# Kernel tuning notes

Hardware: AMD Instinct MI355X
Metric: run time of the kernel (lower is better)

Reference implementation:

```python
import jax, jax.numpy as jnp
import numpy as np


def setup_inputs() -> dict:
    key = jax.random.key(0)
    k1, k2, k3, k4 = jax.random.split(key, 4)
    N, E, DIN, H1, H2 = 100000, 1600000, 128, 64, 32
    x = jax.random.normal(k1, (N, DIN), dtype=jnp.float32)
    edge_index = jax.random.randint(k2, (2, E), 0, N, dtype=jnp.int64)
    # Glorot-style scaled init for the two GCN weight matrices (no bias)
    W1 = jax.random.normal(k3, (DIN, H1), dtype=jnp.float32) * (1.0 / np.sqrt(DIN))
    W2 = jax.random.normal(k4, (H1, H2), dtype=jnp.float32) * (1.0 / np.sqrt(H1))
    return {"x": x, "edge_index": edge_index, "W1": W1, "W2": W2}


def reference(x, edge_index, W1, W2):
    N = x.shape[0]
    loop = jnp.arange(N, dtype=edge_index.dtype)
    src = jnp.concatenate([edge_index[0], loop])  # [E+N]
    dst = jnp.concatenate([edge_index[1], loop])  # [E+N]
    # symmetric GCN normalization with self-loops (edge_weight = 1)
    deg = jax.ops.segment_sum(jnp.ones(src.shape, x.dtype), dst, num_segments=N)
    dinv = jnp.where(deg > 0, jax.lax.rsqrt(deg), 0.0)
    norm = dinv[src] * dinv[dst]  # [E+N]

    def gcn_conv(h, W):
        h = h @ W  # transform first (PyG GCNConv order)
        msg = h[src] * norm[:, None]  # gather + scale
        return jax.ops.segment_sum(msg, dst, num_segments=N)  # scatter-add

    hidden1 = jax.nn.relu(gcn_conv(x, W1))
    z = gcn_conv(hidden1, W2)
    return z
```

## Files before the change

### kernel.cpp

```cpp
#include <hip/hip_runtime.h>
#include <hip/hip_fp16.h>

#define DIN 128
#define H1  64
#define H2  32
#define NCH 512
#define BSH 8

typedef _Float16 f16x8 __attribute__((ext_vector_type(8)));
typedef _Float16 f16x4 __attribute__((ext_vector_type(4)));
typedef float    f32x4 __attribute__((ext_vector_type(4)));

__global__ __launch_bounds__(256) void k_hist(const int* __restrict__ dst,
        int* __restrict__ H, int E, int NB, int chunk) {
    __shared__ int lh[512];
    int c = blockIdx.x, tid = threadIdx.x;
    for (int b = tid; b < NB; b += 256) lh[b] = 0;
    __syncthreads();
    int e0 = c * chunk, e1 = min(E, e0 + chunk);
    for (int e = e0 + tid; e < e1; e += 256)
        atomicAdd(&lh[dst[e] >> BSH], 1);
    __syncthreads();
    for (int b = tid; b < NB; b += 256) H[(size_t)b * NCH + c] = lh[b];
}

__global__ __launch_bounds__(256) void k_scan1(const int* __restrict__ in,
        int* __restrict__ out, int* __restrict__ partial, int N) {
    int tid = threadIdx.x;
    int base = blockIdx.x * 1024 + tid * 4;
    int v0 = (base + 0 < N) ? in[base + 0] : 0;
    int v1 = (base + 1 < N) ? in[base + 1] : 0;
    int v2 = (base + 2 < N) ? in[base + 2] : 0;
    int v3 = (base + 3 < N) ? in[base + 3] : 0;
    int sum = v0 + v1 + v2 + v3;
    int lane = tid & 63, wid = tid >> 6;
    int x = sum;
#pragma unroll
    for (int off = 1; off < 64; off <<= 1) {
        int y = __shfl_up(x, off, 64);
        if (lane >= off) x += y;
    }
    __shared__ int wsum[4];
    if (lane == 63) wsum[wid] = x;
    __syncthreads();
    int wbase = 0;
    for (int w = 0; w < wid; ++w) wbase += wsum[w];
    int excl = wbase + x - sum;
    if (base + 0 < N) out[base + 0] = excl;
    if (base + 1 < N) out[base + 1] = excl + v0;
    if (base + 2 < N) out[base + 2] = excl + v0 + v1;
    if (base + 3 < N) out[base + 3] = excl + v0 + v1 + v2;
    if (tid == 0) partial[blockIdx.x] = wsum[0] + wsum[1] + wsum[2] + wsum[3];
}

__global__ __launch_bounds__(256) void k_scan2(int* __restrict__ partial, int nb) {
    int tid = threadIdx.x;
    int v = (tid < nb) ? partial[tid] : 0;
    __shared__ int tmp[256];
    tmp[tid] = v;
    __syncthreads();
    for (int off = 1; off < 256; off <<= 1) {
        int y = (tid >= off) ? tmp[tid - off] : 0;
        __syncthreads();
        tmp[tid] += y;
        __syncthreads();
    }
    if (tid < nb) partial[tid] = tmp[tid] - v;
}

__global__ void k_scan3b(int* __restrict__ a, const int* __restrict__ partial, int n) {
    int i = blockIdx.x * blockDim.x + threadIdx.x;
    if (i < n) a[i] += partial[i >> 10];
}

__global__ __launch_bounds__(256) void k_bsort(const int* __restrict__ src,
        const int* __restrict__ dst, const int* __restrict__ H,
        int* __restrict__ ep, int E, int NB, int chunk) {
    __shared__ int cur[512];
    int c = blockIdx.x, tid = threadIdx.x;
    for (int b = tid; b < NB; b += 256) cur[b] = H[(size_t)b * NCH + c];
    __syncthreads();
    int e0 = c * chunk, e1 = min(E, e0 + chunk);
    for (int e = e0 + tid; e < e1; e += 256) {
        int s = src[e], d = dst[e];
        int pos = atomicAdd(&cur[d >> BSH], 1);
        ep[pos] = s | ((d & ((1 << BSH) - 1)) << 20);
    }
}

__global__ __launch_bounds__(256) void k_csrA(const int* __restrict__ ep,
        const int* __restrict__ H, int* __restrict__ degi, float* __restrict__ dinv,
        int* __restrict__ lexcl, int* __restrict__ btot, int E, int N, int NB) {
    __shared__ int cnt[256], wsum[4];
    int b = blockIdx.x, tid = threadIdx.x;
    cnt[tid] = 0;
    int bstart = H[(size_t)b * NCH];
    int bend = (b + 1 < NB) ? H[(size_t)(b + 1) * NCH] : E;
    __syncthreads();
    for (int e = bstart + tid; e < bend; e += 256)
        atomicAdd(&cnt[ep[e] >> 20], 1);
    __syncthreads();
    int v = cnt[tid];
    int n = (b << BSH) + tid;
    int d8 = (n < N) ? ((v + 7) & ~7) : 0;
    int lane = tid & 63, wid = tid >> 6;
    int x = d8;
#pragma unroll
    for (int off = 1; off < 64; off <<= 1) {
        int y = __shfl_up(x, off, 64);
        if (lane >= off) x += y;
    }
    if (lane == 63) wsum[wid] = x;
    __syncthreads();
    int wbase = 0;
    for (int w = 0; w < wid; ++w) wbase += wsum[w];
    int excl = wbase + x - d8;
    if (n < N) {
        degi[n]  = v;
        dinv[n]  = rsqrtf((float)v + 1.0f);
        lexcl[n] = excl;
    }
    if (tid == 0) btot[b] = wsum[0] + wsum[1] + wsum[2] + wsum[3];
}

__global__ __launch_bounds__(256) void k_scanC(int* __restrict__ a, int nb) {
    int tid = threadIdx.x;
    int i0 = 2 * tid, i1 = 2 * tid + 1;
    int v0 = (i0 < nb) ? a[i0] : 0;
    int v1 = (i1 < nb) ? a[i1] : 0;
    int p = v0 + v1;
    __shared__ int tmp[256];
    tmp[tid] = p;
    __syncthreads();
    for (int off = 1; off < 256; off <<= 1) {
        int y = (tid >= off) ? tmp[tid - off] : 0;
        __syncthreads();
        tmp[tid] += y;
        __syncthreads();
    }
    int excl = tmp[tid] - p;
    if (i0 < nb) a[i0] = excl;
    if (i1 < nb) a[i1] = excl + v0;
}

__global__ __launch_bounds__(256) void k_csrB(const int* __restrict__ ep,
        const int* __restrict__ H, const int* __restrict__ degi,
        const int* __restrict__ bbase, const int* __restrict__ lexcl,
        int* __restrict__ rowptr, int* __restrict__ csr_src, int E, int N, int NB) {
    __shared__ int pos[256];
    int b = blockIdx.x, tid = threadIdx.x;
    int bstart = H[(size_t)b * NCH];
    int bend = (b + 1 < NB) ? H[(size_t)(b + 1) * NCH] : E;
    int n = (b << BSH) + tid;
    int startv = 0;
    if (n < N) {
        startv = bbase[b] + lexcl[n];
        rowptr[n] = startv;
    }
    pos[tid] = startv;
    __syncthreads();
    for (int e = bstart + tid; e < bend; e += 256) {
        int p = ep[e];
        int q = atomicAdd(&pos[p >> 20], 1);
        csr_src[q] = p & 0xFFFFF;
    }
    __syncthreads();
    if (n < N) {
        int d = degi[n], d8 = (d + 7) & ~7;
        for (int z = startv + d; z < startv + d8; ++z)
            csr_src[z] = N;
    }
}

__global__ __launch_bounds__(256) void k_mgemm1(const float* __restrict__ x,
        const float* __restrict__ W1, const float* __restrict__ dinv,
        _Float16* __restrict__ t1h, int N) {
    __shared__ _Float16 sA[64 * 128];
    __shared__ _Float16 sB[64 * 128];
    int tid = threadIdx.x;
    int row0 = blockIdx.x * 64;
    if (blockIdx.x == 0 && tid < 8)
        ((f32x4*)(t1h + (size_t)N * H1))[tid] = (f32x4){0.f, 0.f, 0.f, 0.f};
#pragma unroll
    for (int i = 0; i < 8; ++i) {
        int idx4 = tid + 256 * i;
        int r = idx4 >> 5, c4 = idx4 & 31;
        int row = row0 + r;
        float4 v = make_float4(0.f, 0.f, 0.f, 0.f);
        if (row < N) v = *(const float4*)&x[(size_t)row * DIN + c4 * 4];
        f16x4 h;
        h[0] = (_Float16)v.x; h[1] = (_Float16)v.y;
        h[2] = (_Float16)v.z; h[3] = (_Float16)v.w;
        int byte = (c4 * 8) ^ ((r & 7) << 4);
        *(f16x4*)((char*)sA + r * 256 + byte) = h;
    }
    {
        int n = tid & 63, kq = tid >> 6;
        _Float16 tmp[32];
#pragma unroll
        for (int kk = 0; kk < 32; ++kk)
            tmp[kk] = (_Float16)W1[(size_t)(kq * 32 + kk) * H1 + n];
#pragma unroll
        for (int j = 0; j < 4; ++j) {
            int byte = ((kq * 32 + j * 8) * 2) ^ ((n & 7) << 4);
            *(f16x8*)((char*)sB + n * 256 + byte) = *(f16x8*)&tmp[j * 8];
        }
    }
    __syncthreads();
    int lane = tid & 63, w = tid >> 6;
    int lr = lane & 15, kg = lane >> 4;
    f32x4 acc[4] = {};
    int ar = w * 16 + lr;
    const char* pa = (const char*)sA + ar * 256;
    int axor = (ar & 7) << 4;
#pragma unroll
    for (int ks = 0; ks < 4; ++ks) {
        int kb = ks * 64 + kg * 16;
        f16x8 a = *(const f16x8*)(pa + (kb ^ axor));
#pragma unroll
        for (int nt = 0; nt < 4; ++nt) {
            int bn = nt * 16 + lr;
            f16x8 b = *(const f16x8*)((const char*)sB + bn * 256 + (kb ^ ((bn & 7) << 4)));
            acc[nt] = __builtin_amdgcn_mfma_f32_16x16x32_f16(a, b, acc[nt], 0, 0, 0);
        }
    }
#pragma unroll
    for (int rg = 0; rg < 4; ++rg) {
        int R = row0 + w * 16 + kg * 4 + rg;
        if (R < N) {
            float dv = dinv[R];
#pragma unroll
            for (int nt = 0; nt < 4; ++nt)
                t1h[(size_t)R * H1 + nt * 16 + lr] = (_Float16)(acc[nt][rg] * dv);
        }
    }
}

__global__ __launch_bounds__(256) void k_mgemm2(const _Float16* __restrict__ aggh,
        const float* __restrict__ W2, const float* __restrict__ dinv,
        _Float16* __restrict__ t2h, int N) {
    __shared__ _Float16 sA[64 * 64];
    __shared__ _Float16 sB[32 * 64];
    int tid = threadIdx.x;
    int row0 = blockIdx.x * 64;
    if (blockIdx.x == 0 && tid < 4)
        ((f32x4*)(t2h + (size_t)N * H2))[tid] = (f32x4){0.f, 0.f, 0.f, 0.f};
#pragma unroll
    for (int i = 0; i < 2; ++i) {
        int idx8 = tid + 256 * i;
        int r = idx8 >> 3, c8 = idx8 & 7;
        int row = row0 + r;
        f16x8 h = {};
        if (row < N) h = *(const f16x8*)&aggh[(size_t)row * H1 + c8 * 8];
        int byte = (c8 * 16) ^ ((r & 7) << 4);
        *(f16x8*)((char*)sA + r * 128 + byte) = h;
    }
    {
        int n = tid & 31, kq = tid >> 5;
        _Float16 tmp[8];
#pragma unroll
        for (int kk = 0; kk < 8; ++kk)
            tmp[kk] = (_Float16)W2[(size_t)(kq * 8 + kk) * H2 + n];
        int byte = (kq * 16) ^ ((n & 7) << 4);
        *(f16x8*)((char*)sB + n * 128 + byte) = *(f16x8*)&tmp[0];
    }
    __syncthreads();
    int lane = tid & 63, w = tid >> 6;
    int lr = lane & 15, kg = lane >> 4;
    f32x4 acc[2] = {};
    int ar = w * 16 + lr;
    const char* pa = (const char*)sA + ar * 128;
    int axor = (ar & 7) << 4;
#pragma unroll
    for (int ks = 0; ks < 2; ++ks) {
        int kb = ks * 64 + kg * 16;
        f16x8 a = *(const f16x8*)(pa + (kb ^ axor));
#pragma unroll
        for (int nt = 0; nt < 2; ++nt) {
            int bn = nt * 16 + lr;
            f16x8 b = *(const f16x8*)((const char*)sB + bn * 128 + (kb ^ ((bn & 7) << 4)));
            acc[nt] = __builtin_amdgcn_mfma_f32_16x16x32_f16(a, b, acc[nt], 0, 0, 0);
        }
    }
#pragma unroll
    for (int rg = 0; rg < 4; ++rg) {
        int R = row0 + w * 16 + kg * 4 + rg;
        if (R < N) {
            float dv = dinv[R];
#pragma unroll
            for (int nt = 0; nt < 2; ++nt)
                t2h[(size_t)R * H2 + nt * 16 + lr] = (_Float16)(acc[nt][rg] * dv);
        }
    }
}

template <int LOGL, bool FUSE>
__global__ __launch_bounds__(256) void k_aggq(const int* __restrict__ rowptr,
        const int* __restrict__ degi, const int* __restrict__ csr_src,
        const float* __restrict__ dinv, const _Float16* __restrict__ tp,
        void* __restrict__ outv, int N) {
    const int L = 1 << LOGL;
    const int F = L * 8;
    int local = threadIdx.x >> LOGL;
    int j = threadIdx.x & (L - 1);
    int n = blockIdx.x * (256 >> LOGL) + local;
    if (n >= N) return;
    int start = rowptr[n];
    int deg = degi[n];
    f16x8 sv = *(const f16x8*)&tp[(size_t)n * F + j * 8];
    float acc[8];
#pragma unroll
    for (int t = 0; t < 8; ++t) acc[t] = (float)sv[t];
    for (int k = 0; k < deg; k += 8) {
        int4 ra = *(const int4*)&csr_src[start + k];
        int4 rb = *(const int4*)&csr_src[start + k + 4];
        int idx[8] = {ra.x, ra.y, ra.z, ra.w, rb.x, rb.y, rb.z, rb.w};
        f16x8 g[8];
#pragma unroll
        for (int u = 0; u < 8; ++u)
            g[u] = *(const f16x8*)&tp[(size_t)idx[u] * F + j * 8];
#pragma unroll
        for (int u = 0; u < 8; ++u)
#pragma unroll
            for (int t = 0; t < 8; ++t)
                acc[t] += (float)g[u][t];
    }
    float dv = dinv[n];
    if (FUSE) {
        f16x8 o;
#pragma unroll
        for (int t = 0; t < 8; ++t) o[t] = (_Float16)fmaxf(acc[t] * dv, 0.f);
        *(f16x8*)((_Float16*)outv + (size_t)n * F + j * 8) = o;
    } else {
        float* op = (float*)outv + (size_t)n * F + j * 8;
        f32x4 o0 = {acc[0] * dv, acc[1] * dv, acc[2] * dv, acc[3] * dv};
        f32x4 o1 = {acc[4] * dv, acc[5] * dv, acc[6] * dv, acc[7] * dv};
        *(f32x4*)op = o0;
        *(f32x4*)(op + 4) = o1;
    }
}

extern "C" void kernel_launch(void* const* d_in, const int* in_sizes, int n_in,
                              void* d_out, int out_size, void* d_ws, size_t ws_size,
                              hipStream_t stream) {
    const float* x  = (const float*)d_in[0];
    const int*   ei = (const int*)d_in[1];
    const float* W1 = (const float*)d_in[2];
    const float* W2 = (const float*)d_in[3];

    const int N = in_sizes[0] / DIN;
    const int E = in_sizes[1] / 2;
    const int* src = ei;
    const int* dst = ei + E;

    const int NB    = (N + (1 << BSH) - 1) >> BSH;
    const int NBNCH = NB * NCH;
    const int chunk = (E + NCH - 1) / NCH;

    float*    dinv    = (float*)d_ws;
    int*      degi    = (int*)(dinv + N);
    int*      rowptr  = degi + N;
    int*      lexcl   = rowptr + N;
    int*      H       = lexcl + N;
    int*      partial = H + NBNCH;
    int*      btot    = partial + 256;
    int*      csr_src = btot + 512;
    _Float16* t1h     = (_Float16*)(csr_src + E + 8 * N);
    _Float16* agg1h   = t1h + (size_t)(N + 1) * H1;
    _Float16* t2h     = t1h;
    float*    out     = (float*)d_out;
    int*      ep      = (int*)t1h;

    k_hist<<<NCH, 256, 0, stream>>>(dst, H, E, NB, chunk);
    k_scan1<<<(NBNCH + 1023) / 1024, 256, 0, stream>>>(H, H, partial, NBNCH);
    k_scan2<<<1, 256, 0, stream>>>(partial, (NBNCH + 1023) / 1024);
    k_scan3b<<<(NBNCH + 255) / 256, 256, 0, stream>>>(H, partial, NBNCH);
    k_bsort<<<NCH, 256, 0, stream>>>(src, dst, H, ep, E, NB, chunk);
    k_csrA<<<NB, 256, 0, stream>>>(ep, H, degi, dinv, lexcl, btot, E, N, NB);
    k_scanC<<<1, 256, 0, stream>>>(btot, NB);
    k_csrB<<<NB, 256, 0, stream>>>(ep, H, degi, btot, lexcl, rowptr, csr_src, E, N, NB);

    const int ntile = (N + 63) / 64;

    k_mgemm1<<<ntile, 256, 0, stream>>>(x, W1, dinv, t1h, N);
    k_aggq<3, true><<<(N + 31) / 32, 256, 0, stream>>>(rowptr, degi, csr_src, dinv,
                                                       t1h, agg1h, N);

    k_mgemm2<<<ntile, 256, 0, stream>>>(agg1h, W2, dinv, t2h, N);
    k_aggq<2, false><<<(N + 63) / 64, 256, 0, stream>>>(rowptr, degi, csr_src, dinv,
                                                        t2h, out, N);
}
```

Baseline: 128.5 us.

## Fuse CSR build kernels and fold scan fixup into consumers

```diff
diff --git a/kernel.cpp b/kernel.cpp
--- a/kernel.cpp
+++ b/kernel.cpp
@@ -4,7 +4,7 @@
 #define DIN 128
 #define H1  64
 #define H2  32
-#define NCH 512
+#define NCH 256
 #define BSH 8
 
 typedef _Float16 f16x8 __attribute__((ext_vector_type(8)));
@@ -68,17 +68,16 @@
     if (tid < nb) partial[tid] = tmp[tid] - v;
 }
 
-__global__ void k_scan3b(int* __restrict__ a, const int* __restrict__ partial, int n) {
-    int i = blockIdx.x * blockDim.x + threadIdx.x;
-    if (i < n) a[i] += partial[i >> 10];
-}
-
 __global__ __launch_bounds__(256) void k_bsort(const int* __restrict__ src,
         const int* __restrict__ dst, const int* __restrict__ H,
-        int* __restrict__ ep, int E, int NB, int chunk) {
+        const int* __restrict__ partial, int* __restrict__ ep,
+        int E, int NB, int chunk) {
     __shared__ int cur[512];
     int c = blockIdx.x, tid = threadIdx.x;
-    for (int b = tid; b < NB; b += 256) cur[b] = H[(size_t)b * NCH + c];
+    for (int b = tid; b < NB; b += 256) {
+        int idx = b * NCH + c;
+        cur[b] = H[idx] + partial[idx >> 10];
+    }
     __syncthreads();
     int e0 = c * chunk, e1 = min(E, e0 + chunk);
     for (int e = e0 + tid; e < e1; e += 256) {
@@ -88,14 +87,21 @@
     }
 }
 
-__global__ __launch_bounds__(256) void k_csrA(const int* __restrict__ ep,
-        const int* __restrict__ H, int* __restrict__ degi, float* __restrict__ dinv,
-        int* __restrict__ lexcl, int* __restrict__ btot, int E, int N, int NB) {
-    __shared__ int cnt[256], wsum[4];
+__global__ __launch_bounds__(256) void k_csr(const int* __restrict__ ep,
+        const int* __restrict__ H, const int* __restrict__ partial,
+        int* __restrict__ degi, int* __restrict__ rowptr, float* __restrict__ dinv,
+        int* __restrict__ csr_src, int E, int N, int NB) {
+    __shared__ int cnt[256], pos[256], wsum[4];
     int b = blockIdx.x, tid = threadIdx.x;
     cnt[tid] = 0;
-    int bstart = H[(size_t)b * NCH];
-    int bend = (b + 1 < NB) ? H[(size_t)(b + 1) * NCH] : E;
+    int i0 = b * NCH;
+    int bstart = H[i0] + partial[i0 >> 10];
+    int bend = E;
+    if (b + 1 < NB) {
+        int i1 = (b + 1) * NCH;
+        bend = H[i1] + partial[i1 >> 10];
+    }
+    int base8 = (bstart + b * 2048 + 7) & ~7;
     __syncthreads();
     for (int e = bstart + tid; e < bend; e += 256)
         atomicAdd(&cnt[ep[e] >> 20], 1);
@@ -114,47 +120,10 @@
     __syncthreads();
     int wbase = 0;
     for (int w = 0; w < wid; ++w) wbase += wsum[w];
-    int excl = wbase + x - d8;
+    int startv = base8 + wbase + x - d8;
     if (n < N) {
-        degi[n]  = v;
-        dinv[n]  = rsqrtf((float)v + 1.0f);
-        lexcl[n] = excl;
-    }
-    if (tid == 0) btot[b] = wsum[0] + wsum[1] + wsum[2] + wsum[3];
-}
-
-__global__ __launch_bounds__(256) void k_scanC(int* __restrict__ a, int nb) {
-    int tid = threadIdx.x;
-    int i0 = 2 * tid, i1 = 2 * tid + 1;
-    int v0 = (i0 < nb) ? a[i0] : 0;
-    int v1 = (i1 < nb) ? a[i1] : 0;
-    int p = v0 + v1;
-    __shared__ int tmp[256];
-    tmp[tid] = p;
-    __syncthreads();
-    for (int off = 1; off < 256; off <<= 1) {
-        int y = (tid >= off) ? tmp[tid - off] : 0;
-        __syncthreads();
-        tmp[tid] += y;
-        __syncthreads();
-    }
-    int excl = tmp[tid] - p;
-    if (i0 < nb) a[i0] = excl;
-    if (i1 < nb) a[i1] = excl + v0;
-}
-
-__global__ __launch_bounds__(256) void k_csrB(const int* __restrict__ ep,
-        const int* __restrict__ H, const int* __restrict__ degi,
-        const int* __restrict__ bbase, const int* __restrict__ lexcl,
-        int* __restrict__ rowptr, int* __restrict__ csr_src, int E, int N, int NB) {
-    __shared__ int pos[256];
-    int b = blockIdx.x, tid = threadIdx.x;
-    int bstart = H[(size_t)b * NCH];
-    int bend = (b + 1 < NB) ? H[(size_t)(b + 1) * NCH] : E;
-    int n = (b << BSH) + tid;
-    int startv = 0;
-    if (n < N) {
-        startv = bbase[b] + lexcl[n];
+        degi[n]   = v;
+        dinv[n]   = rsqrtf((float)v + 1.0f);
         rowptr[n] = startv;
     }
     pos[tid] = startv;
@@ -166,8 +135,8 @@
     }
     __syncthreads();
     if (n < N) {
-        int d = degi[n], d8 = (d + 7) & ~7;
-        for (int z = startv + d; z < startv + d8; ++z)
+        int d = degi[n], dd8 = (d + 7) & ~7;
+        for (int z = startv + d; z < startv + dd8; ++z)
             csr_src[z] = N;
     }
 }
@@ -360,12 +329,10 @@
     float*    dinv    = (float*)d_ws;
     int*      degi    = (int*)(dinv + N);
     int*      rowptr  = degi + N;
-    int*      lexcl   = rowptr + N;
-    int*      H       = lexcl + N;
+    int*      H       = rowptr + N;
     int*      partial = H + NBNCH;
-    int*      btot    = partial + 256;
-    int*      csr_src = btot + 512;
-    _Float16* t1h     = (_Float16*)(csr_src + E + 8 * N);
+    int*      csr_src = partial + 256;
+    _Float16* t1h     = (_Float16*)(csr_src + E + 2048 * NB + 8);
     _Float16* agg1h   = t1h + (size_t)(N + 1) * H1;
     _Float16* t2h     = t1h;
     float*    out     = (float*)d_out;
@@ -374,11 +341,8 @@
     k_hist<<<NCH, 256, 0, stream>>>(dst, H, E, NB, chunk);
     k_scan1<<<(NBNCH + 1023) / 1024, 256, 0, stream>>>(H, H, partial, NBNCH);
     k_scan2<<<1, 256, 0, stream>>>(partial, (NBNCH + 1023) / 1024);
-    k_scan3b<<<(NBNCH + 255) / 256, 256, 0, stream>>>(H, partial, NBNCH);
-    k_bsort<<<NCH, 256, 0, stream>>>(src, dst, H, ep, E, NB, chunk);
-    k_csrA<<<NB, 256, 0, stream>>>(ep, H, degi, dinv, lexcl, btot, E, N, NB);
-    k_scanC<<<1, 256, 0, stream>>>(btot, NB);
-    k_csrB<<<NB, 256, 0, stream>>>(ep, H, degi, btot, lexcl, rowptr, csr_src, E, N, NB);
+    k_bsort<<<NCH, 256, 0, stream>>>(src, dst, H, partial, ep, E, NB, chunk);
+    k_csr<<<NB, 256, 0, stream>>>(ep, H, partial, degi, rowptr, dinv, csr_src, E, N, NB);
 
     const int ntile = (N + 63) / 64;
 
```

Result: slower. 145.3 us (+13.0%).

## Split feature matrices into 16-column slabs and aggregate per slab

Applied to the files above, without the earlier changes.

```diff
diff --git a/kernel.cpp b/kernel.cpp
--- a/kernel.cpp
+++ b/kernel.cpp
@@ -179,8 +179,11 @@
     __shared__ _Float16 sB[64 * 128];
     int tid = threadIdx.x;
     int row0 = blockIdx.x * 64;
-    if (blockIdx.x == 0 && tid < 8)
-        ((f32x4*)(t1h + (size_t)N * H1))[tid] = (f32x4){0.f, 0.f, 0.f, 0.f};
+    if (blockIdx.x == 0 && tid < 8) {
+        int q = tid >> 1, hh = tid & 1;
+        *(f32x4*)(t1h + (size_t)q * (N + 1) * 16 + (size_t)N * 16 + hh * 8) =
+            (f32x4){0.f, 0.f, 0.f, 0.f};
+    }
 #pragma unroll
     for (int i = 0; i < 8; ++i) {
         int idx4 = tid + 256 * i;
@@ -231,7 +234,8 @@
             float dv = dinv[R];
 #pragma unroll
             for (int nt = 0; nt < 4; ++nt)
-                t1h[(size_t)R * H1 + nt * 16 + lr] = (_Float16)(acc[nt][rg] * dv);
+                t1h[(size_t)nt * (N + 1) * 16 + (size_t)R * 16 + lr] =
+                    (_Float16)(acc[nt][rg] * dv);
         }
     }
 }
@@ -243,15 +247,21 @@
     __shared__ _Float16 sB[32 * 64];
     int tid = threadIdx.x;
     int row0 = blockIdx.x * 64;
-    if (blockIdx.x == 0 && tid < 4)
-        ((f32x4*)(t2h + (size_t)N * H2))[tid] = (f32x4){0.f, 0.f, 0.f, 0.f};
+    if (blockIdx.x == 0 && tid < 4) {
+        int q = tid >> 1, hh = tid & 1;
+        *(f32x4*)(t2h + (size_t)q * (N + 1) * 16 + (size_t)N * 16 + hh * 8) =
+            (f32x4){0.f, 0.f, 0.f, 0.f};
+    }
 #pragma unroll
     for (int i = 0; i < 2; ++i) {
         int idx8 = tid + 256 * i;
         int r = idx8 >> 3, c8 = idx8 & 7;
         int row = row0 + r;
         f16x8 h = {};
-        if (row < N) h = *(const f16x8*)&aggh[(size_t)row * H1 + c8 * 8];
+        if (row < N) {
+            int q = c8 >> 1, h8 = c8 & 1;
+            h = *(const f16x8*)&aggh[(size_t)q * (N + 1) * 16 + (size_t)row * 16 + h8 * 8];
+        }
         int byte = (c8 * 16) ^ ((r & 7) << 4);
         *(f16x8*)((char*)sA + r * 128 + byte) = h;
     }
@@ -289,25 +299,26 @@
             float dv = dinv[R];
 #pragma unroll
             for (int nt = 0; nt < 2; ++nt)
-                t2h[(size_t)R * H2 + nt * 16 + lr] = (_Float16)(acc[nt][rg] * dv);
-        }
-    }
-}
-
-template <int LOGL, bool FUSE>
-__global__ __launch_bounds__(256) void k_aggq(const int* __restrict__ rowptr,
+                t2h[(size_t)nt * (N + 1) * 16 + (size_t)R * 16 + lr] =
+                    (_Float16)(acc[nt][rg] * dv);
+        }
+    }
+}
+
+template <bool FUSE>
+__global__ __launch_bounds__(256) void k_aggf(const int* __restrict__ rowptr,
         const int* __restrict__ degi, const int* __restrict__ csr_src,
         const float* __restrict__ dinv, const _Float16* __restrict__ tp,
         void* __restrict__ outv, int N) {
-    const int L = 1 << LOGL;
-    const int F = L * 8;
-    int local = threadIdx.x >> LOGL;
-    int j = threadIdx.x & (L - 1);
-    int n = blockIdx.x * (256 >> LOGL) + local;
+    int q = blockIdx.y;
+    const _Float16* tq = tp + (size_t)q * (N + 1) * 16;
+    int local = threadIdx.x >> 1;
+    int j = threadIdx.x & 1;
+    int n = blockIdx.x * 128 + local;
     if (n >= N) return;
     int start = rowptr[n];
     int deg = degi[n];
-    f16x8 sv = *(const f16x8*)&tp[(size_t)n * F + j * 8];
+    f16x8 sv = *(const f16x8*)&tq[(size_t)n * 16 + j * 8];
     float acc[8];
 #pragma unroll
     for (int t = 0; t < 8; ++t) acc[t] = (float)sv[t];
@@ -318,7 +329,7 @@
         f16x8 g[8];
 #pragma unroll
         for (int u = 0; u < 8; ++u)
-            g[u] = *(const f16x8*)&tp[(size_t)idx[u] * F + j * 8];
+            g[u] = *(const f16x8*)&tq[(size_t)idx[u] * 16 + j * 8];
 #pragma unroll
         for (int u = 0; u < 8; ++u)
 #pragma unroll
@@ -330,9 +341,9 @@
         f16x8 o;
 #pragma unroll
         for (int t = 0; t < 8; ++t) o[t] = (_Float16)fmaxf(acc[t] * dv, 0.f);
-        *(f16x8*)((_Float16*)outv + (size_t)n * F + j * 8) = o;
+        *(f16x8*)((_Float16*)outv + (size_t)q * (N + 1) * 16 + (size_t)n * 16 + j * 8) = o;
     } else {
-        float* op = (float*)outv + (size_t)n * F + j * 8;
+        float* op = (float*)outv + (size_t)n * 32 + q * 16 + j * 8;
         f32x4 o0 = {acc[0] * dv, acc[1] * dv, acc[2] * dv, acc[3] * dv};
         f32x4 o1 = {acc[4] * dv, acc[5] * dv, acc[6] * dv, acc[7] * dv};
         *(f32x4*)op = o0;
@@ -381,12 +392,17 @@
     k_csrB<<<NB, 256, 0, stream>>>(ep, H, degi, btot, lexcl, rowptr, csr_src, E, N, NB);
 
     const int ntile = (N + 63) / 64;
+    const int nblk  = (N + 127) / 128;
 
     k_mgemm1<<<ntile, 256, 0, stream>>>(x, W1, dinv, t1h, N);
-    k_aggq<3, true><<<(N + 31) / 32, 256, 0, stream>>>(rowptr, degi, csr_src, dinv,
-                                                       t1h, agg1h, N);
+    {
+        dim3 g(nblk, 4);
+        k_aggf<true><<<g, 256, 0, stream>>>(rowptr, degi, csr_src, dinv, t1h, agg1h, N);
+    }
 
     k_mgemm2<<<ntile, 256, 0, stream>>>(agg1h, W2, dinv, t2h, N);
-    k_aggq<2, false><<<(N + 63) / 64, 256, 0, stream>>>(rowptr, degi, csr_src, dinv,
-                                                        t2h, out, N);
-}
+    {
+        dim3 g(nblk, 2);
+        k_aggf<false><<<g, 256, 0, stream>>>(rowptr, degi, csr_src, dinv, t2h, out, N);
+    }
+}
```

After: 157.3 us. 22.3% more time.

## Sort nodes by degree bucket for balanced aggregation work per wavefront

Applied to the files above, without the earlier changes.

```diff
diff --git a/kernel.cpp b/kernel.cpp
--- a/kernel.cpp
+++ b/kernel.cpp
@@ -172,6 +172,40 @@
     }
 }
 
+__global__ __launch_bounds__(256) void k_dhist(const int* __restrict__ degi,
+        int* __restrict__ DH, int N, int NBLK) {
+    __shared__ int lh[64];
+    int blk = blockIdx.x, tid = threadIdx.x;
+    if (tid < 64) lh[tid] = 0;
+    __syncthreads();
+    int base = blk * 1024;
+    for (int i = tid; i < 1024; i += 256) {
+        int n = base + i;
+        if (n < N) atomicAdd(&lh[min((degi[n] + 7) >> 3, 63)], 1);
+    }
+    __syncthreads();
+    if (tid < 64) DH[(size_t)tid * NBLK + blk] = lh[tid];
+}
+
+__global__ __launch_bounds__(256) void k_dscat(const int* __restrict__ degi,
+        const int* __restrict__ rowptr, const float* __restrict__ dinv,
+        const int* __restrict__ DH, int4* __restrict__ pk, int N, int NBLK) {
+    __shared__ int cur[64];
+    int blk = blockIdx.x, tid = threadIdx.x;
+    if (tid < 64) cur[tid] = DH[(size_t)tid * NBLK + blk];
+    __syncthreads();
+    int base = blk * 1024;
+    for (int i = tid; i < 1024; i += 256) {
+        int n = base + i;
+        if (n < N) {
+            int d = degi[n];
+            int c = min((d + 7) >> 3, 63);
+            int pos = atomicAdd(&cur[c], 1);
+            pk[pos] = make_int4(rowptr[n], d, __float_as_int(dinv[n]), n);
+        }
+    }
+}
+
 __global__ __launch_bounds__(256) void k_mgemm1(const float* __restrict__ x,
         const float* __restrict__ W1, const float* __restrict__ dinv,
         _Float16* __restrict__ t1h, int N) {
@@ -295,18 +329,20 @@
 }
 
 template <int LOGL, bool FUSE>
-__global__ __launch_bounds__(256) void k_aggq(const int* __restrict__ rowptr,
-        const int* __restrict__ degi, const int* __restrict__ csr_src,
-        const float* __restrict__ dinv, const _Float16* __restrict__ tp,
+__global__ __launch_bounds__(256) void k_aggq(const int4* __restrict__ pk,
+        const int* __restrict__ csr_src, const _Float16* __restrict__ tp,
         void* __restrict__ outv, int N) {
     const int L = 1 << LOGL;
     const int F = L * 8;
     int local = threadIdx.x >> LOGL;
     int j = threadIdx.x & (L - 1);
-    int n = blockIdx.x * (256 >> LOGL) + local;
-    if (n >= N) return;
-    int start = rowptr[n];
-    int deg = degi[n];
+    int i = blockIdx.x * (256 >> LOGL) + local;
+    if (i >= N) return;
+    int4 p = pk[i];
+    int start = p.x;
+    int deg = p.y;
+    float dv = __int_as_float(p.z);
+    int n = p.w;
     f16x8 sv = *(const f16x8*)&tp[(size_t)n * F + j * 8];
     float acc[8];
 #pragma unroll
@@ -325,7 +361,6 @@
             for (int t = 0; t < 8; ++t)
                 acc[t] += (float)g[u][t];
     }
-    float dv = dinv[n];
     if (FUSE) {
         f16x8 o;
 #pragma unroll
@@ -356,6 +391,7 @@
     const int NB    = (N + (1 << BSH) - 1) >> BSH;
     const int NBNCH = NB * NCH;
     const int chunk = (E + NCH - 1) / NCH;
+    const int NBLK  = (N + 1023) / 1024;
 
     float*    dinv    = (float*)d_ws;
     int*      degi    = (int*)(dinv + N);
@@ -364,7 +400,10 @@
     int*      H       = lexcl + N;
     int*      partial = H + NBNCH;
     int*      btot    = partial + 256;
-    int*      csr_src = btot + 512;
+    int*      DH      = btot + 512;
+    int*      dpart   = DH + 64 * NBLK;
+    int4*     pk      = (int4*)(dpart + 64);
+    int*      csr_src = (int*)(pk + N);
     _Float16* t1h     = (_Float16*)(csr_src + E + 8 * N);
     _Float16* agg1h   = t1h + (size_t)(N + 1) * H1;
     _Float16* t2h     = t1h;
@@ -380,13 +419,20 @@
     k_scanC<<<1, 256, 0, stream>>>(btot, NB);
     k_csrB<<<NB, 256, 0, stream>>>(ep, H, degi, btot, lexcl, rowptr, csr_src, E, N, NB);
 
+    {
+        const int DHT = 64 * NBLK;
+        k_dhist<<<NBLK, 256, 0, stream>>>(degi, DH, N, NBLK);
+        k_scan1<<<(DHT + 1023) / 1024, 256, 0, stream>>>(DH, DH, dpart, DHT);
+        k_scan2<<<1, 256, 0, stream>>>(dpart, (DHT + 1023) / 1024);
+        k_scan3b<<<(DHT + 255) / 256, 256, 0, stream>>>(DH, dpart, DHT);
+        k_dscat<<<NBLK, 256, 0, stream>>>(degi, rowptr, dinv, DH, pk, N, NBLK);
+    }
+
     const int ntile = (N + 63) / 64;
 
     k_mgemm1<<<ntile, 256, 0, stream>>>(x, W1, dinv, t1h, N);
-    k_aggq<3, true><<<(N + 31) / 32, 256, 0, stream>>>(rowptr, degi, csr_src, dinv,
-                                                       t1h, agg1h, N);
+    k_aggq<3, true><<<(N + 31) / 32, 256, 0, stream>>>(pk, csr_src, t1h, agg1h, N);
 
     k_mgemm2<<<ntile, 256, 0, stream>>>(agg1h, W2, dinv, t2h, N);
-    k_aggq<2, false><<<(N + 63) / 64, 256, 0, stream>>>(rowptr, degi, csr_src, dinv,
-                                                        t2h, out, N);
-}
+    k_aggq<2, false><<<(N + 63) / 64, 256, 0, stream>>>(pk, csr_src, t2h, out, N);
+}
```

After: 143.0 us. +11.2%, slower.
